# Kernel tuning notes

Hardware: AMD Instinct MI355X
Metric: run time of the kernel (lower is better)

## Reference

```python
import jax, jax.numpy as jnp
import numpy as np

N = 20000      # nodes
E = 320000     # edges (avg degree 16)
IN, HID, OUT, H = 128, 32, 32, 8
NEG_SLOPE = 0.2


def _gat_conv(x, src, dst, W, al, ar, b):
    """One DGL-style GATConv. x: [N, F_in], W: [F_in, H*D], al/ar: [H, D], b: [H*D].
    Returns [N, H, D]."""
    n = x.shape[0]
    Hh, D = al.shape
    feat = (x @ W).reshape(n, Hh, D)                      # [N,H,D]
    el = jnp.sum(feat * al[None], axis=-1)                # [N,H]
    er = jnp.sum(feat * ar[None], axis=-1)                # [N,H]
    e = jax.nn.leaky_relu(el[src] + er[dst], NEG_SLOPE)   # [E,H]
    # edge softmax over incoming edges of each dst node (stable)
    emax = jax.ops.segment_max(e, dst, num_segments=n)    # [N,H]
    ee = jnp.exp(e - emax[dst])                           # [E,H]
    denom = jax.ops.segment_sum(ee, dst, num_segments=n)  # [N,H]
    alpha = ee / denom[dst]                               # [E,H]
    msg = feat[src] * alpha[:, :, None]                   # [E,H,D] gather+weight
    out = jax.ops.segment_sum(msg, dst, num_segments=n)   # [N,H,D] scatter-add
    return out + b.reshape(1, Hh, D)


def setup_inputs() -> dict:
    key = jax.random.key(0)
    ks = jax.random.split(key, 11)
    return {
        "x":   jax.random.normal(ks[0], (N, IN), dtype=jnp.float32),
        "src": jax.random.randint(ks[1], (E,), 0, N, dtype=jnp.int32),
        "dst": jax.random.randint(ks[2], (E,), 0, N, dtype=jnp.int32),
        "W1":  jax.random.normal(ks[3], (IN, H * HID), dtype=jnp.float32) * 0.1,
        "al1": jax.random.normal(ks[4], (H, HID), dtype=jnp.float32) * 0.1,
        "ar1": jax.random.normal(ks[5], (H, HID), dtype=jnp.float32) * 0.1,
        "b1":  jnp.zeros((H * HID,), dtype=jnp.float32),
        "W2":  jax.random.normal(ks[6], (HID, H * OUT), dtype=jnp.float32) * 0.1,
        "al2": jax.random.normal(ks[7], (H, OUT), dtype=jnp.float32) * 0.1,
        "ar2": jax.random.normal(ks[8], (H, OUT), dtype=jnp.float32) * 0.1,
        "b2":  jnp.zeros((H * OUT,), dtype=jnp.float32),
    }


def reference(x, src, dst, W1, al1, ar1, b1, W2, al2, ar2, b2):
    h = _gat_conv(x, src, dst, W1, al1, ar1, b1)          # [N,H,HID]
    h = jnp.mean(jax.nn.relu(h), axis=1)                  # [N,HID]
    h = _gat_conv(h, src, dst, W2, al2, ar2, b2)          # [N,H,OUT]
    return jnp.mean(h, axis=1)                            # [N,OUT]
```

## Files before the change

### kernel.cpp

```cpp
#include <hip/hip_runtime.h>
#include <hip/hip_bf16.h>

#define N_NODES 20000
#define N_EDGES 320000
#define F_IN    128
#define F_HID   32
#define NHEAD   8
#define FDIM    256
#define CAP     96

#define GROUPS  313
#define GCAP    2048
#define EPB     2048
#define P1B     ((N_EDGES + EPB - 1) / EPB)

typedef __hip_bfloat16 bf16;
typedef __attribute__((ext_vector_type(8))) short short8;
typedef __attribute__((ext_vector_type(4))) float f32x4;

__device__ __forceinline__ unsigned short f2bf_rne(float f){
  unsigned u = __float_as_uint(f);
  unsigned r = u + 0x7FFFu + ((u >> 16) & 1u);
  return (unsigned short)(r >> 16);
}
__device__ __forceinline__ float bf2f(unsigned short s){
  return __uint_as_float((unsigned)s << 16);
}

__global__ void init_kernel(const float* __restrict__ W1, const float* __restrict__ W2,
                            const float* __restrict__ al2, const float* __restrict__ ar2,
                            int* __restrict__ gcnt,
                            unsigned short* __restrict__ h1, unsigned short* __restrict__ l1,
                            float* __restrict__ q_lt, float* __restrict__ q_rt){
  const int b = blockIdx.x;
  if (b == 0){
    for (int i = threadIdx.x; i < GROUPS; i += 256) gcnt[i] = 0;
  } else if (b < 129){
    int i = (b - 1)*256 + threadIdx.x;
    int n = i >> 7, k = i & 127;
    float v = W1[(size_t)k*FDIM + n];
    unsigned short hs = f2bf_rne(v);
    h1[i] = hs;
    l1[i] = f2bf_rne(v - bf2f(hs));
  } else {
    int t = threadIdx.x;
    int k = t >> 3, hh = t & 7;
    float sl = 0.f, sr = 0.f;
    #pragma unroll
    for (int d = 0; d < 32; d++){
      float w = W2[(size_t)k*FDIM + hh*32 + d];
      sl = fmaf(w, al2[hh*32 + d], sl);
      sr = fmaf(w, ar2[hh*32 + d], sr);
    }
    q_lt[t] = sl;
    q_rt[t] = sr;
  }
}

#define GEMMB  (N_NODES / 16)
__global__ __launch_bounds__(256) void gemm_p1_kernel(
    const int* __restrict__ src, const int* __restrict__ dst,
    int* __restrict__ gcnt, unsigned* __restrict__ recs,
    const float* __restrict__ X,
    const unsigned short* __restrict__ Wthi, const unsigned short* __restrict__ Wtlo,
    const float* __restrict__ al, const float* __restrict__ ar,
    unsigned short* __restrict__ feat, float* __restrict__ el, float* __restrict__ er)
{
  const int b = blockIdx.x;
  const int tid = threadIdx.x;

  if (b < P1B){
    __shared__ int hist[GROUPS];
    for (int t = tid; t < GROUPS; t += 256) hist[t] = 0;
    __syncthreads();

    unsigned rec[8]; int bin[8]; bool val[8];
    const int e0 = b * EPB;
    #pragma unroll
    for (int k = 0; k < 8; k++){
      int i = e0 + k*256 + tid;
      val[k] = (i < N_EDGES);
      if (val[k]){
        int s = src[i];
        int d = dst[i];
        bin[k] = d >> 6;
        rec[k] = (unsigned)(((d & 63) << 16) | s);
        atomicAdd(&hist[bin[k]], 1);
      }
    }
    __syncthreads();
    for (int t = tid; t < GROUPS; t += 256){
      int h = hist[t];
      hist[t] = (h > 0) ? atomicAdd(&gcnt[t], h) : 0;
    }
    __syncthreads();
    #pragma unroll
    for (int k = 0; k < 8; k++){
      if (val[k]){
        int pos = atomicAdd(&hist[bin[k]], 1);
        if (pos < GCAP) recs[(size_t)bin[k]*GCAP + pos] = rec[k];
      }
    }
    return;
  }

  constexpr int K = F_IN;
  const int wv   = tid >> 6;
  const int lane = tid & 63;
  const int quad = lane >> 4;
  const int l16  = lane & 15;
  const int m0   = (b - P1B) * 16;
  constexpr int NC = K / 32;

  short8 Ah[NC], Al_[NC];
  {
    const float* xrow = X + (size_t)(m0 + l16)*K;
    #pragma unroll
    for (int c = 0; c < NC; c++){
      float4 a0 = *(const float4*)(xrow + c*32 + quad*8);
      float4 a1 = *(const float4*)(xrow + c*32 + quad*8 + 4);
      const float vs[8] = {a0.x,a0.y,a0.z,a0.w,a1.x,a1.y,a1.z,a1.w};
      #pragma unroll
      for (int j = 0; j < 8; j++){
        unsigned short hs = f2bf_rne(vs[j]);
        Ah[c][j]  = (short)hs;
        Al_[c][j] = (short)f2bf_rne(vs[j] - bf2f(hs));
      }
    }
  }

  float elp[8], erp[8];
  #pragma unroll
  for (int j = 0; j < 8; j++){ elp[j] = 0.f; erp[j] = 0.f; }

  #pragma unroll
  for (int t = 0; t < 4; t++){
    const int nc = wv*64 + t*16;
    const size_t brow = (size_t)(nc + l16) * K;
    f32x4 acc = {0.f, 0.f, 0.f, 0.f};
    #pragma unroll
    for (int c = 0; c < NC; c++){
      short8 Bh = *(const short8*)(Wthi + brow + c*32 + quad*8);
      short8 Bl = *(const short8*)(Wtlo + brow + c*32 + quad*8);
      acc = __builtin_amdgcn_mfma_f32_16x16x32_bf16(Ah[c],  Bh, acc, 0, 0, 0);
      acc = __builtin_amdgcn_mfma_f32_16x16x32_bf16(Ah[c],  Bl, acc, 0, 0, 0);
      acc = __builtin_amdgcn_mfma_f32_16x16x32_bf16(Al_[c], Bh, acc, 0, 0, 0);
    }
    const float alv = al[nc + l16];
    const float arv = ar[nc + l16];
    const int hl = t >> 1;
    #pragma unroll
    for (int r = 0; r < 4; r++){
      float v = acc[r];
      feat[(size_t)(m0 + quad*4 + r)*FDIM + nc + l16] = f2bf_rne(v);
      elp[r*2 + hl] = fmaf(v, alv, elp[r*2 + hl]);
      erp[r*2 + hl] = fmaf(v, arv, erp[r*2 + hl]);
    }
  }

  #pragma unroll
  for (int off = 1; off <= 8; off <<= 1){
    #pragma unroll
    for (int j = 0; j < 8; j++){
      elp[j] += __shfl_xor(elp[j], off);
      erp[j] += __shfl_xor(erp[j], off);
    }
  }
  __shared__ float el_lds[16][8], er_lds[16][8];
  if (l16 == 0){
    #pragma unroll
    for (int r = 0; r < 4; r++){
      #pragma unroll
      for (int hl = 0; hl < 2; hl++){
        el_lds[quad*4 + r][wv*2 + hl] = elp[r*2 + hl];
        er_lds[quad*4 + r][wv*2 + hl] = erp[r*2 + hl];
      }
    }
  }
  __syncthreads();
  if (tid < 128){
    int row = tid >> 3, h = tid & 7;
    el[(size_t)(m0 + row)*NHEAD + h] = el_lds[row][h];
    er[(size_t)(m0 + row)*NHEAD + h] = er_lds[row][h];
  }
}

__global__ __launch_bounds__(256) void bucket_build_kernel(
    const unsigned* __restrict__ recs, const int* __restrict__ gcnt,
    int* __restrict__ cnt, int* __restrict__ bucket)
{
  const int g  = blockIdx.x;
  const int n0 = g << 6;
  __shared__ int lcnt[64];
  __shared__ int lbuck[64*CAP];
  if (threadIdx.x < 64) lcnt[threadIdx.x] = 0;
  __syncthreads();

  int m = gcnt[g]; if (m > GCAP) m = GCAP;
  for (int r = threadIdx.x; r < m; r += 256){
    unsigned w = recs[(size_t)g*GCAP + r];
    int d = (int)(w >> 16);
    int p = atomicAdd(&lcnt[d], 1);
    if (p < CAP) lbuck[d*CAP + p] = (int)(w & 0xFFFFu);
  }
  __syncthreads();

  int nn = N_NODES - n0; if (nn > 64) nn = 64;
  if (threadIdx.x < nn) cnt[n0 + threadIdx.x] = lcnt[threadIdx.x];
  const int tot4 = (nn * CAP) >> 2;
  int4* gb = (int4*)(bucket + (size_t)n0 * CAP);
  const int4* lb = (const int4*)lbuck;
  for (int i = threadIdx.x; i < tot4; i += 256) gb[i] = lb[i];
}

__global__ __launch_bounds__(256) void edge_agg_l1(
    const bf16* __restrict__ feat, const float* __restrict__ el,
    const float* __restrict__ er, const int* __restrict__ cnt,
    const int* __restrict__ bucket, const float* __restrict__ bias,
    const float* __restrict__ q_lt, const float* __restrict__ q_rt,
    unsigned short* __restrict__ h_out, float* __restrict__ el2,
    float* __restrict__ er2)
{
  const int tid  = threadIdx.x;
  const int wv   = tid >> 6;
  const int lane = tid & 63;
  const int n    = blockIdx.x*4 + wv;

  __shared__ float t_all[4][CAP*9];
  __shared__ int   s_all[4][CAP];
  __shared__ float sum_all[4][NHEAD];
  __shared__ float v_all[4][256];
  float* t_w = t_all[wv];
  int*   s_w = s_all[wv];

  int C = cnt[n];
  if (C > CAP) C = CAP;

  const float4* er4 = (const float4*)(er + (size_t)n*NHEAD);
  float4 era = er4[0], erb = er4[1];
  const float erv[8] = {era.x, era.y, era.z, era.w, erb.x, erb.y, erb.z, erb.w};

  for (int idx = lane; idx < C*2; idx += 64){
    const int e = idx >> 1, j = idx & 1;
    const int sidx = bucket[(size_t)n*CAP + e];
    if (j == 0) s_w[e] = sidx;
    float4 a = ((const float4*)(el + (size_t)sidx*NHEAD))[j];
    const float ev[4] = {a.x, a.y, a.z, a.w};
    #pragma unroll
    for (int hh = 0; hh < 4; hh++){
      float v = ev[hh] + erv[j*4 + hh];
      t_w[e*9 + j*4 + hh] = (v > 0.f) ? v : 0.2f*v;
    }
  }
  {
    const int h = lane >> 3, d = lane & 7;
    float lm = -INFINITY;
    for (int e = d; e < C; e += 8) lm = fmaxf(lm, t_w[e*9 + h]);
    #pragma unroll
    for (int off = 4; off >= 1; off >>= 1) lm = fmaxf(lm, __shfl_xor(lm, off));
    float ls = 0.f;
    for (int e = d; e < C; e += 8){
      float ex = __expf(t_w[e*9 + h] - lm);
      t_w[e*9 + h] = ex;
      ls += ex;
    }
    #pragma unroll
    for (int off = 4; off >= 1; off >>= 1) ls += __shfl_xor(ls, off);
    if (d == 0) sum_all[wv][h] = ls;
  }

  const int sub = lane >> 5;
  const int l   = lane & 31;
  const int hB  = l >> 2;
  const int coff = l << 3;
  float acc[8] = {0,0,0,0,0,0,0,0};
  int e = sub;
  float4 fv;
  if (e < C) fv = *(const float4*)(feat + (size_t)s_w[e]*FDIM + coff);
  while (e < C){
    const int en = e + 2;
    float4 fnext;
    if (en < C) fnext = *(const float4*)(feat + (size_t)s_w[en]*FDIM + coff);
    const float w = t_w[e*9 + hB];
    const unsigned* u = (const unsigned*)&fv;
    #pragma unroll
    for (int j = 0; j < 4; j++){
      float flo = __uint_as_float(u[j] << 16);
      float fhi = __uint_as_float(u[j] & 0xFFFF0000u);
      acc[2*j]   = fmaf(w, flo, acc[2*j]);
      acc[2*j+1] = fmaf(w, fhi, acc[2*j+1]);
    }
    fv = fnext;
    e = en;
  }
  #pragma unroll
  for (int j = 0; j < 8; j++) acc[j] += __shfl_xor(acc[j], 32);

  if (lane < 32){
    const float s = sum_all[wv][l >> 2];
    const float4* b4 = (const float4*)(bias + coff);
    float4 ba = b4[0], bb = b4[1];
    float bv[8] = {ba.x, ba.y, ba.z, ba.w, bb.x, bb.y, bb.z, bb.w};
    float v[8];
    #pragma unroll
    for (int j = 0; j < 8; j++){
      float val = (C > 0) ? (acc[j] / s) : 0.f;
      val += bv[j];
      val = fmaxf(val, 0.f);
      v[j] = val;
    }
    float4* v4 = (float4*)&v_all[wv][coff];
    v4[0] = make_float4(v[0], v[1], v[2], v[3]);
    v4[1] = make_float4(v[4], v[5], v[6], v[7]);
  }
  if (lane < 32){
    float hsum = 0.f;
    #pragma unroll
    for (int hh = 0; hh < 8; hh++) hsum += v_all[wv][hh*32 + lane];
    hsum *= 0.125f;
    h_out[(size_t)n*32 + lane] = f2bf_rne(hsum);

    float4 qa0 = ((const float4*)(q_lt + lane*8))[0];
    float4 qa1 = ((const float4*)(q_lt + lane*8))[1];
    float4 qb0 = ((const float4*)(q_rt + lane*8))[0];
    float4 qb1 = ((const float4*)(q_rt + lane*8))[1];
    float pl[8] = {hsum*qa0.x, hsum*qa0.y, hsum*qa0.z, hsum*qa0.w,
                   hsum*qa1.x, hsum*qa1.y, hsum*qa1.z, hsum*qa1.w};
    float pr[8] = {hsum*qb0.x, hsum*qb0.y, hsum*qb0.z, hsum*qb0.w,
                   hsum*qb1.x, hsum*qb1.y, hsum*qb1.z, hsum*qb1.w};
    #pragma unroll
    for (int off = 1; off <= 16; off <<= 1){
      #pragma unroll
      for (int j = 0; j < 8; j++){
        pl[j] += __shfl_xor(pl[j], off);
        pr[j] += __shfl_xor(pr[j], off);
      }
    }
    if (l == 0){
      #pragma unroll
      for (int j = 0; j < 8; j++){
        el2[(size_t)n*NHEAD + j] = pl[j];
        er2[(size_t)n*NHEAD + j] = pr[j];
      }
    }
  }
}

__global__ __launch_bounds__(256) void edge_agg_l2(
    const unsigned short* __restrict__ h_bf, const float* __restrict__ el2,
    const float* __restrict__ er2, const int* __restrict__ cnt,
    const int* __restrict__ bucket, const float* __restrict__ W2,
    const float* __restrict__ b2, float* __restrict__ outp)
{
  const int tid  = threadIdx.x;
  const int wv   = tid >> 6;
  const int lane = tid & 63;
  const int n    = blockIdx.x*4 + wv;

  __shared__ float t_all[4][CAP*9];
  __shared__ int   s_all[4][CAP];
  __shared__ float sum_all[4][NHEAD];
  __shared__ float A_lds[4][NHEAD][33];
  __shared__ float red[4][256];
  float* t_w = t_all[wv];
  int*   s_w = s_all[wv];

  int C = cnt[n];
  if (C > CAP) C = CAP;

  const float4* er4 = (const float4*)(er2 + (size_t)n*NHEAD);
  float4 era = er4[0], erb = er4[1];
  const float erv[8] = {era.x, era.y, era.z, era.w, erb.x, erb.y, erb.z, erb.w};

  for (int idx = lane; idx < C*2; idx += 64){
    const int e = idx >> 1, j = idx & 1;
    const int sidx = bucket[(size_t)n*CAP + e];
    if (j == 0) s_w[e] = sidx;
    float4 a = ((const float4*)(el2 + (size_t)sidx*NHEAD))[j];
    const float ev[4] = {a.x, a.y, a.z, a.w};
    #pragma unroll
    for (int hh = 0; hh < 4; hh++){
      float v = ev[hh] + erv[j*4 + hh];
      t_w[e*9 + j*4 + hh] = (v > 0.f) ? v : 0.2f*v;
    }
  }
  {
    const int h = lane >> 3, d = lane & 7;
    float lm = -INFINITY;
    for (int e = d; e < C; e += 8) lm = fmaxf(lm, t_w[e*9 + h]);
    #pragma unroll
    for (int off = 4; off >= 1; off >>= 1) lm = fmaxf(lm, __shfl_xor(lm, off));
    float ls = 0.f;
    for (int e = d; e < C; e += 8){
      float ex = __expf(t_w[e*9 + h] - lm);
      t_w[e*9 + h] = ex;
      ls += ex;
    }
    #pragma unroll
    for (int off = 4; off >= 1; off >>= 1) ls += __shfl_xor(ls, off);
    if (d == 0) sum_all[wv][h] = ls;
  }

  const int h  = lane & 7;
  const int dg = lane >> 3;
  float A0=0.f, A1=0.f, A2=0.f, A3=0.f;
  int e = 0;
  ushort4 hv;
  if (e < C) hv = *(const ushort4*)(h_bf + (size_t)s_w[e]*32 + dg*4);
  while (e < C){
    const int en = e + 1;
    ushort4 hnext;
    if (en < C) hnext = *(const ushort4*)(h_bf + (size_t)s_w[en]*32 + dg*4);
    const float w = t_w[e*9 + h];
    A0 = fmaf(w, bf2f(hv.x), A0);
    A1 = fmaf(w, bf2f(hv.y), A1);
    A2 = fmaf(w, bf2f(hv.z), A2);
    A3 = fmaf(w, bf2f(hv.w), A3);
    hv = hnext;
    e = en;
  }
  {
    const float s = sum_all[wv][h];
    const float inv = (C > 0) ? (1.f / s) : 0.f;
    A_lds[wv][h][dg*4 + 0] = A0 * inv;
    A_lds[wv][h][dg*4 + 1] = A1 * inv;
    A_lds[wv][h][dg*4 + 2] = A2 * inv;
    A_lds[wv][h][dg*4 + 3] = A3 * inv;
  }
  __syncthreads();

  {
    const int c  = tid;
    const int hc = c >> 5;
    float p0=0.f, p1=0.f, p2=0.f, p3=0.f;
    for (int k = 0; k < F_HID; k++){
      float w = W2[(size_t)k*FDIM + c];
      p0 = fmaf(A_lds[0][hc][k], w, p0);
      p1 = fmaf(A_lds[1][hc][k], w, p1);
      p2 = fmaf(A_lds[2][hc][k], w, p2);
      p3 = fmaf(A_lds[3][hc][k], w, p3);
    }
    red[0][c] = p0; red[1][c] = p1; red[2][c] = p2; red[3][c] = p3;
  }
  __syncthreads();
  if (tid < 128){
    const int nn = tid >> 5, d = tid & 31;
    float s = 0.f, bm = 0.f;
    #pragma unroll
    for (int hh = 0; hh < 8; hh++){
      s  += red[nn][hh*32 + d];
      bm += b2[hh*32 + d];
    }
    outp[(size_t)(blockIdx.x*4 + nn)*32 + d] = (s + bm) * 0.125f;
  }
}

extern "C" void kernel_launch(void* const* d_in, const int* in_sizes, int n_in,
                              void* d_out, int out_size, void* d_ws, size_t ws_size,
                              hipStream_t stream)
{
  const float* x   = (const float*)d_in[0];
  const int*   src = (const int*)  d_in[1];
  const int*   dst = (const int*)  d_in[2];
  const float* W1  = (const float*)d_in[3];
  const float* al1 = (const float*)d_in[4];
  const float* ar1 = (const float*)d_in[5];
  const float* b1  = (const float*)d_in[6];
  const float* W2  = (const float*)d_in[7];
  const float* al2 = (const float*)d_in[8];
  const float* ar2 = (const float*)d_in[9];
  const float* b2  = (const float*)d_in[10];
  (void)in_sizes; (void)n_in; (void)out_size; (void)ws_size;

  size_t o = 0;
  char* base = (char*)d_ws;
  auto take = [&](size_t bytes) -> char* {
    char* p = base + o;
    o += (bytes + 255) & ~(size_t)255;
    return p;
  };
  unsigned short* feat  = (unsigned short*)take((size_t)N_NODES*FDIM*2);
  float* el1    = (float*)take((size_t)N_NODES*NHEAD*4);
  float* er1    = (float*)take((size_t)N_NODES*NHEAD*4);
  float* el2    = (float*)take((size_t)N_NODES*NHEAD*4);
  float* er2    = (float*)take((size_t)N_NODES*NHEAD*4);
  int*   cnt    = (int*)  take((size_t)N_NODES*4);
  int*   bucket = (int*)  take((size_t)N_NODES*CAP*4);
  unsigned short* hbf  = (unsigned short*)take((size_t)N_NODES*F_HID*2);
  unsigned short* W1th = (unsigned short*)take((size_t)FDIM*F_IN*2);
  unsigned short* W1tl = (unsigned short*)take((size_t)FDIM*F_IN*2);
  float* q_lt   = (float*)take((size_t)F_HID*NHEAD*4);
  float* q_rt   = (float*)take((size_t)F_HID*NHEAD*4);
  int*   gcnt   = (int*)  take((size_t)GROUPS*4);
  unsigned* recs = (unsigned*)take((size_t)GROUPS*GCAP*4);

  init_kernel<<<130, 256, 0, stream>>>(
      W1, W2, al2, ar2, gcnt, W1th, W1tl, q_lt, q_rt);

  gemm_p1_kernel<<<P1B + GEMMB, 256, 0, stream>>>(
      src, dst, gcnt, recs, x, W1th, W1tl, al1, ar1, feat, el1, er1);

  bucket_build_kernel<<<GROUPS, 256, 0, stream>>>(recs, gcnt, cnt, bucket);

  edge_agg_l1<<<N_NODES/4, 256, 0, stream>>>(
      (const bf16*)feat, el1, er1, cnt, bucket, b1, q_lt, q_rt, hbf, el2, er2);

  edge_agg_l2<<<N_NODES/4, 256, 0, stream>>>(
      hbf, el2, er2, cnt, bucket, W2, b2, (float*)d_out);
}
```

Baseline: 187.8 us.

## Pad group counters, deepen layer-1 prefetch, restructure layer-2 edge aggregation

Group counters are padded to separate 64-byte lines, and each partition block visits them in a rotated order to spread global atomic contention. The layer-1 aggregation loop now keeps two feature rows in flight instead of one to hide gather latency. The layer-2 aggregation is remapped so each lane covers two feature columns for all eight heads across four parallel edge streams. Attention weights are read as vector loads from a 12-float padded LDS row, followed by a cross-lane shuffle reduction. This trades extra registers and shuffles for fewer, wider loads and more memory-level parallelism.

```diff
diff --git a/kernel.cpp b/kernel.cpp
--- a/kernel.cpp
+++ b/kernel.cpp
@@ -10,9 +10,12 @@
 #define CAP     96
 
 #define GROUPS  313
+#define GPAD    16
 #define GCAP    2048
 #define EPB     2048
 #define P1B     ((N_EDGES + EPB - 1) / EPB)
+
+#define TW2     12
 
 typedef __hip_bfloat16 bf16;
 typedef __attribute__((ext_vector_type(8))) short short8;
@@ -34,7 +37,7 @@
                             float* __restrict__ q_lt, float* __restrict__ q_rt){
   const int b = blockIdx.x;
   if (b == 0){
-    for (int i = threadIdx.x; i < GROUPS; i += 256) gcnt[i] = 0;
+    for (int i = threadIdx.x; i < GROUPS*GPAD; i += 256) gcnt[i] = 0;
   } else if (b < 129){
     int i = (b - 1)*256 + threadIdx.x;
     int n = i >> 7, k = i & 127;
@@ -89,9 +92,13 @@
       }
     }
     __syncthreads();
-    for (int t = tid; t < GROUPS; t += 256){
-      int h = hist[t];
-      hist[t] = (h > 0) ? atomicAdd(&gcnt[t], h) : 0;
+    {
+      const int rot = (b * 97) % GROUPS;
+      for (int tt = tid; tt < GROUPS; tt += 256){
+        int t = tt + rot; if (t >= GROUPS) t -= GROUPS;
+        int h = hist[t];
+        hist[t] = (h > 0) ? atomicAdd(&gcnt[t*GPAD], h) : 0;
+      }
     }
     __syncthreads();
     #pragma unroll
@@ -196,7 +203,7 @@
   if (threadIdx.x < 64) lcnt[threadIdx.x] = 0;
   __syncthreads();
 
-  int m = gcnt[g]; if (m > GCAP) m = GCAP;
+  int m = gcnt[g*GPAD]; if (m > GCAP) m = GCAP;
   for (int r = threadIdx.x; r < m; r += 256){
     unsigned w = recs[(size_t)g*GCAP + r];
     int d = (int)(w >> 16);
@@ -275,14 +282,14 @@
   const int coff = l << 3;
   float acc[8] = {0,0,0,0,0,0,0,0};
   int e = sub;
-  float4 fv;
-  if (e < C) fv = *(const float4*)(feat + (size_t)s_w[e]*FDIM + coff);
+  float4 fv0, fv1;
+  if (e < C)     fv0 = *(const float4*)(feat + (size_t)s_w[e]*FDIM + coff);
+  if (e + 2 < C) fv1 = *(const float4*)(feat + (size_t)s_w[e+2]*FDIM + coff);
   while (e < C){
-    const int en = e + 2;
     float4 fnext;
-    if (en < C) fnext = *(const float4*)(feat + (size_t)s_w[en]*FDIM + coff);
+    if (e + 4 < C) fnext = *(const float4*)(feat + (size_t)s_w[e+4]*FDIM + coff);
     const float w = t_w[e*9 + hB];
-    const unsigned* u = (const unsigned*)&fv;
+    const unsigned* u = (const unsigned*)&fv0;
     #pragma unroll
     for (int j = 0; j < 4; j++){
       float flo = __uint_as_float(u[j] << 16);
@@ -290,8 +297,8 @@
       acc[2*j]   = fmaf(w, flo, acc[2*j]);
       acc[2*j+1] = fmaf(w, fhi, acc[2*j+1]);
     }
-    fv = fnext;
-    e = en;
+    fv0 = fv1; fv1 = fnext;
+    e += 2;
   }
   #pragma unroll
   for (int j = 0; j < 8; j++) acc[j] += __shfl_xor(acc[j], 32);
@@ -357,7 +364,7 @@
   const int lane = tid & 63;
   const int n    = blockIdx.x*4 + wv;
 
-  __shared__ float t_all[4][CAP*9];
+  __shared__ __align__(16) float t_all[4][CAP*TW2];
   __shared__ int   s_all[4][CAP];
   __shared__ float sum_all[4][NHEAD];
   __shared__ float A_lds[4][NHEAD][33];
@@ -381,19 +388,19 @@
     #pragma unroll
     for (int hh = 0; hh < 4; hh++){
       float v = ev[hh] + erv[j*4 + hh];
-      t_w[e*9 + j*4 + hh] = (v > 0.f) ? v : 0.2f*v;
+      t_w[e*TW2 + j*4 + hh] = (v > 0.f) ? v : 0.2f*v;
     }
   }
   {
     const int h = lane >> 3, d = lane & 7;
     float lm = -INFINITY;
-    for (int e = d; e < C; e += 8) lm = fmaxf(lm, t_w[e*9 + h]);
+    for (int e = d; e < C; e += 8) lm = fmaxf(lm, t_w[e*TW2 + h]);
     #pragma unroll
     for (int off = 4; off >= 1; off >>= 1) lm = fmaxf(lm, __shfl_xor(lm, off));
     float ls = 0.f;
     for (int e = d; e < C; e += 8){
-      float ex = __expf(t_w[e*9 + h] - lm);
-      t_w[e*9 + h] = ex;
+      float ex = __expf(t_w[e*TW2 + h] - lm);
+      t_w[e*TW2 + h] = ex;
       ls += ex;
     }
     #pragma unroll
@@ -401,31 +408,45 @@
     if (d == 0) sum_all[wv][h] = ls;
   }
 
-  const int h  = lane & 7;
-  const int dg = lane >> 3;
-  float A0=0.f, A1=0.f, A2=0.f, A3=0.f;
-  int e = 0;
-  ushort4 hv;
-  if (e < C) hv = *(const ushort4*)(h_bf + (size_t)s_w[e]*32 + dg*4);
+  const int sub = lane >> 4;
+  const int q   = lane & 15;
+  float acc[16];
+  #pragma unroll
+  for (int i = 0; i < 16; i++) acc[i] = 0.f;
+  int e = sub;
+  unsigned hv;
+  if (e < C) hv = *(const unsigned*)(h_bf + (size_t)s_w[e]*32 + q*2);
   while (e < C){
-    const int en = e + 1;
-    ushort4 hnext;
-    if (en < C) hnext = *(const ushort4*)(h_bf + (size_t)s_w[en]*32 + dg*4);
-    const float w = t_w[e*9 + h];
-    A0 = fmaf(w, bf2f(hv.x), A0);
-    A1 = fmaf(w, bf2f(hv.y), A1);
-    A2 = fmaf(w, bf2f(hv.z), A2);
-    A3 = fmaf(w, bf2f(hv.w), A3);
+    const int en = e + 4;
+    unsigned hnext;
+    if (en < C) hnext = *(const unsigned*)(h_bf + (size_t)s_w[en]*32 + q*2);
+    f32x4 w0 = *(const f32x4*)&t_w[e*TW2];
+    f32x4 w1 = *(const f32x4*)&t_w[e*TW2 + 4];
+    const float x0 = __uint_as_float(hv << 16);
+    const float x1 = __uint_as_float(hv & 0xFFFF0000u);
+    #pragma unroll
+    for (int h = 0; h < 4; h++){
+      acc[2*h]   = fmaf(w0[h], x0, acc[2*h]);
+      acc[2*h+1] = fmaf(w0[h], x1, acc[2*h+1]);
+      acc[8+2*h]   = fmaf(w1[h], x0, acc[8+2*h]);
+      acc[8+2*h+1] = fmaf(w1[h], x1, acc[8+2*h+1]);
+    }
     hv = hnext;
     e = en;
   }
-  {
-    const float s = sum_all[wv][h];
-    const float inv = (C > 0) ? (1.f / s) : 0.f;
-    A_lds[wv][h][dg*4 + 0] = A0 * inv;
-    A_lds[wv][h][dg*4 + 1] = A1 * inv;
-    A_lds[wv][h][dg*4 + 2] = A2 * inv;
-    A_lds[wv][h][dg*4 + 3] = A3 * inv;
+  #pragma unroll
+  for (int i = 0; i < 16; i++){
+    acc[i] += __shfl_xor(acc[i], 16);
+    acc[i] += __shfl_xor(acc[i], 32);
+  }
+  if (lane < 16){
+    #pragma unroll
+    for (int h = 0; h < 8; h++){
+      const float s = sum_all[wv][h];
+      const float inv = (C > 0) ? (1.f / s) : 0.f;
+      A_lds[wv][h][2*lane]     = acc[2*h]   * inv;
+      A_lds[wv][h][2*lane + 1] = acc[2*h+1] * inv;
+    }
   }
   __syncthreads();
 
@@ -491,7 +512,7 @@
   unsigned short* W1tl = (unsigned short*)take((size_t)FDIM*F_IN*2);
   float* q_lt   = (float*)take((size_t)F_HID*NHEAD*4);
   float* q_rt   = (float*)take((size_t)F_HID*NHEAD*4);
-  int*   gcnt   = (int*)  take((size_t)GROUPS*4);
+  int*   gcnt   = (int*)  take((size_t)GROUPS*GPAD*4);
   unsigned* recs = (unsigned*)take((size_t)GROUPS*GCAP*4);
 
   init_kernel<<<130, 256, 0, stream>>>(
```

Result: faster. 182.9 us (-2.6%).
